# Performance work log

Measured on AMD Instinct MI355X. Metric: run time of the kernel, lower is better.

Reference implementation:

```python
import jax, jax.numpy as jnp
import numpy as np

DN = ('NCHW', 'OIHW', 'NCHW')

def _conv(x, w, b, pad):
    y = jax.lax.conv_general_dilated(x, w, (1, 1), pad, dimension_numbers=DN)
    return y + b[None, :, None, None]

def setup_inputs() -> dict:
    key = jax.random.key(0)
    ks = jax.random.split(key, 8)
    B, C, H, W = 8, 256, 64, 64
    C8 = C // 8
    return {
        'x': jax.random.normal(ks[0], (B, C, H, W), jnp.float32),
        'wq': jax.random.normal(ks[1], (C8, C, 1, 3), jnp.float32) * 0.02,
        'bq': jax.random.normal(ks[2], (C8,), jnp.float32) * 0.02,
        'wk': jax.random.normal(ks[3], (C8, C, 3, 1), jnp.float32) * 0.02,
        'bk': jax.random.normal(ks[4], (C8,), jnp.float32) * 0.02,
        'wv': jax.random.normal(ks[5], (C, C, 1, 1), jnp.float32) * 0.02,
        'bv': jax.random.normal(ks[6], (C,), jnp.float32) * 0.02,
        'gamma': jax.random.normal(ks[7], (1,), jnp.float32),
    }

def reference(x, wq, bq, wk, bk, wv, bv, gamma):
    B, C, H, W = x.shape
    N = H * W
    # q: (1,3) kernel, pad (0,1); k: (3,1) kernel, pad (1,0); v: 1x1
    q = _conv(x, wq, bq, [(0, 0), (1, 1)]).reshape(B, -1, N)  # B, C/8, N
    k = _conv(x, wk, bk, [(1, 1), (0, 0)]).reshape(B, -1, N)  # B, C/8, N
    v = _conv(x, wv, bv, [(0, 0), (0, 0)]).reshape(B, C, N)   # B, C, N
    affinity = jnp.einsum('bci,bcj->bij', q, k)               # B, N, N
    affinity = jax.nn.softmax(affinity, axis=-1)
    # weights = v @ affinity^T  ->  (B, C, N)
    weights = jnp.einsum('bcj,bij->bci', v, affinity).reshape(B, C, H, W)
    return gamma[0] * weights + x
```

## Files before the change

### kernel.cpp

```cpp
#include <hip/hip_runtime.h>
#include <math.h>

#define LOG2E 1.44269504f

typedef unsigned short us;
typedef __attribute__((ext_vector_type(8))) short bf16x8;
typedef __attribute__((ext_vector_type(4))) float f32x4;
typedef __attribute__((ext_vector_type(16))) float f32x16;

static __device__ __forceinline__ us f2bf(float f) {
  union { float f; unsigned u; } v; v.f = f;
  unsigned r = v.u + 0x7fffu + ((v.u >> 16) & 1u);
  return (us)(r >> 16);
}

__global__ __launch_bounds__(256) void prep_kernel(
    const float* __restrict__ x, const float* __restrict__ wq,
    const float* __restrict__ wk, const float* __restrict__ wv,
    us* __restrict__ xT, us* __restrict__ wqc, us* __restrict__ wkc,
    us* __restrict__ wvb) {
  __shared__ __align__(16) us lt[64 * 68];
  int bid = blockIdx.x;
  int tid = threadIdx.x;
  if (bid < 2048) {
    int b = bid >> 8, cb = (bid >> 6) & 3, nb = bid & 63;
    const float* xb = x + (((size_t)(b * 256 + cb * 64)) << 12);
    int nl = tid & 63, ch = tid >> 6;
#pragma unroll
    for (int p = 0; p < 16; p++) {
      int c = p * 4 + ch;
      lt[nl * 68 + c] = f2bf(xb[((size_t)c << 12) + (nb * 64 + nl)]);
    }
    __syncthreads();
    us* xTb = xT + (((size_t)b << 12) + nb * 64) * 256 + cb * 64;
    int cw = tid & 7, nr0 = tid >> 3;
#pragma unroll
    for (int p2 = 0; p2 < 2; p2++) {
      int nr = p2 * 32 + nr0;
      uint2 lo = *(const uint2*)&lt[nr * 68 + cw * 8];
      uint2 hi = *(const uint2*)&lt[nr * 68 + cw * 8 + 4];
      *(uint4*)&xTb[(size_t)nr * 256 + cw * 8] = make_uint4(lo.x, lo.y, hi.x, hi.y);
    }
  } else {
    int idx = (bid - 2048) * 256 + tid;
    if (idx < 24576) {
      int oc = idx / 768, r = idx % 768, t = r >> 8, ic = r & 255;
      wqc[idx] = f2bf(wq[(oc * 256 + ic) * 3 + t] * LOG2E);
    } else if (idx < 49152) {
      int j = idx - 24576;
      int oc = j / 768, r = j % 768, t = r >> 8, ic = r & 255;
      wkc[j] = f2bf(wk[(oc * 256 + ic) * 3 + t]);
    } else if (idx < 114688) {
      int j = idx - 49152;
      wvb[j] = f2bf(wv[j]);
    }
  }
}

__global__ __launch_bounds__(256) void conv_kernel(
    const us* __restrict__ xT, const us* __restrict__ wqc,
    const us* __restrict__ wkc, const float* __restrict__ bq,
    const float* __restrict__ bk, const us* __restrict__ wvb,
    const float* __restrict__ bv, us* __restrict__ qT, us* __restrict__ kT,
    us* __restrict__ vblk) {
  int tid = threadIdx.x, lane = tid & 63, w = tid >> 6;
  int l15 = lane & 15, quad = lane >> 4;
  if (blockIdx.x < 512) {
    int bid = blockIdx.x;
    int b = bid & 7, rt = bid >> 3;
    int n0 = rt * 64, y = rt;
    bool isq = (w < 2);
    int m0 = (w & 1) * 16;
    const us* wc = isq ? wqc : wkc;
    const us* xTb = xT + (((size_t)b << 12) * 256);
    f32x4 acc[4];
#pragma unroll
    for (int nt = 0; nt < 4; nt++) acc[nt] = (f32x4){0.f, 0.f, 0.f, 0.f};
#pragma unroll
    for (int t = 0; t < 3; t++) {
      bool killT = (!isq) && ((t == 0 && y == 0) || (t == 2 && y == 63));
      if (!killT) {
        int dn = isq ? (t - 1) : (t - 1) * 64;
#pragma unroll
        for (int k8 = 0; k8 < 8; k8++) {
          int kloc = t * 256 + k8 * 32 + quad * 8;
          bf16x8 af = *(const bf16x8*)(wc + (size_t)(m0 + l15) * 768 + kloc);
          int ic = k8 * 32 + quad * 8;
#pragma unroll
          for (int nt = 0; nt < 4; nt++) {
            int nl = nt * 16 + l15;
            int ns = n0 + nl + dn;
            ns = ns < 0 ? 0 : (ns > 4095 ? 4095 : ns);
            bf16x8 bf = *(const bf16x8*)(xTb + (size_t)ns * 256 + ic);
            if (isq && ((t == 0 && nl == 0) || (t == 2 && nl == 63)))
              bf = (bf16x8){0, 0, 0, 0, 0, 0, 0, 0};
            acc[nt] = __builtin_amdgcn_mfma_f32_16x16x32_bf16(af, bf, acc[nt], 0, 0, 0);
          }
        }
      }
    }
    const float* bias = isq ? bq : bk;
    float bsc = isq ? LOG2E : 1.0f;
    us* outp = (isq ? qT : kT) + (((size_t)b << 12) * 32);
    float b0 = bias[m0 + quad * 4 + 0] * bsc;
    float b1 = bias[m0 + quad * 4 + 1] * bsc;
    float b2 = bias[m0 + quad * 4 + 2] * bsc;
    float b3 = bias[m0 + quad * 4 + 3] * bsc;
#pragma unroll
    for (int nt = 0; nt < 4; nt++) {
      int n = n0 + nt * 16 + l15;
      unsigned lo = (unsigned)f2bf(acc[nt][0] + b0) | ((unsigned)f2bf(acc[nt][1] + b1) << 16);
      unsigned hi = (unsigned)f2bf(acc[nt][2] + b2) | ((unsigned)f2bf(acc[nt][3] + b3) << 16);
      *(uint2*)(outp + (size_t)n * 32 + m0 + quad * 4) = make_uint2(lo, hi);
    }
  } else {
    int bid = blockIdx.x - 512;
    int b = bid & 7, nt0 = bid >> 3;
    int n0 = nt0 * 64;
    const us* xTb = xT + (((size_t)b << 12) * 256);
    f32x4 acc[4][4];
#pragma unroll
    for (int ct = 0; ct < 4; ct++)
#pragma unroll
      for (int nt = 0; nt < 4; nt++) acc[ct][nt] = (f32x4){0.f, 0.f, 0.f, 0.f};
#pragma unroll
    for (int kk = 0; kk < 8; kk++) {
      bf16x8 bfr[4];
#pragma unroll
      for (int nt = 0; nt < 4; nt++)
        bfr[nt] = *(const bf16x8*)(xTb + (size_t)(n0 + nt * 16 + l15) * 256 + kk * 32 + quad * 8);
#pragma unroll
      for (int ct = 0; ct < 4; ct++) {
        bf16x8 af = *(const bf16x8*)(wvb + (size_t)(w * 64 + ct * 16 + l15) * 256 + kk * 32 + quad * 8);
#pragma unroll
        for (int nt = 0; nt < 4; nt++)
          acc[ct][nt] = __builtin_amdgcn_mfma_f32_16x16x32_bf16(af, bfr[nt], acc[ct][nt], 0, 0, 0);
      }
    }
    us* vb = vblk + ((size_t)b << 20);
#pragma unroll
    for (int ct = 0; ct < 4; ct++) {
#pragma unroll
      for (int r = 0; r < 4; r++) {
        int oc = w * 64 + ct * 16 + quad * 4 + r;
        float bvv = bv[oc];
#pragma unroll
        for (int nt = 0; nt < 4; nt++) {
          vb[((size_t)((n0 >> 4) + nt) * 256 + oc) * 16 + l15] = f2bf(acc[ct][nt][r] + bvv);
        }
      }
    }
  }
}

__global__ __launch_bounds__(512, 8) void attn_kernel(
    const float* __restrict__ x, const us* __restrict__ qT,
    const us* __restrict__ kT, const us* __restrict__ vblk,
    const float* __restrict__ gamma_p, float* __restrict__ out) {
  __shared__ __align__(16) us pb[2][32 * 72];
  __shared__ float lpart[4][32];

  int tid = threadIdx.x, lane = tid & 63, w = tid >> 6;
  int l15 = lane & 15, quad = lane >> 4;
  int l31 = lane & 31, h32 = lane >> 5;
  int iw = w & 1, jq = w >> 1;

  int bid = blockIdx.x;
  int b = bid & 7, i0 = (bid >> 3) * 32;

  const us* qTb = qT + (((size_t)b << 12) * 32);
  const us* kTb = kT + (((size_t)b << 12) * 32);
  const us* vbb = vblk + ((size_t)b << 20);

  bf16x8 qf = *(const bf16x8*)(qTb + (size_t)(i0 + iw * 16 + l15) * 32 + quad * 8);

  const us* kbase = kTb + (size_t)(jq * 16 + l15) * 32 + quad * 8;
  const us* vbase = vbb + (size_t)(w * 32 + l31) * 16 + h32 * 8;
  int pwi = (iw * 16 + l15) * 72 + jq * 16 + quad * 4;
  int pri = l31 * 72 + h32 * 8;

  float lr = 0.f;
  f32x4 s;
  f32x16 o;
#pragma unroll
  for (int rg = 0; rg < 16; rg++) o[rg] = 0.f;

  bf16x8 kX, kY;
  bf16x8 vf0, vf1, vf2, vf3;

#define PREK(N, KD)                                                            \
  do { KD = *(const bf16x8*)(kbase + (size_t)((N) & 63) * 2048); } while (0)

#define PREV(N)                                                                \
  do {                                                                         \
    const us* vp = vbase + (size_t)((N) & 63) * 16384;                         \
    vf0 = *(const bf16x8*)(vp);                                                \
    vf1 = *(const bf16x8*)(vp + 4096);                                         \
    vf2 = *(const bf16x8*)(vp + 8192);                                         \
    vf3 = *(const bf16x8*)(vp + 12288);                                        \
  } while (0)

#define STEP(N, KC, KN, BUF)                                                   \
  do {                                                                         \
    __builtin_amdgcn_s_setprio(1);                                             \
    s = __builtin_amdgcn_mfma_f32_16x16x32_bf16(KC, qf, (f32x4){0.f, 0.f, 0.f, 0.f}, 0, 0, 0); \
    __builtin_amdgcn_s_setprio(0);                                             \
    PREV(N);                                                                   \
    PREK((N) + 1, KN);                                                         \
    {                                                                          \
      float p0 = __builtin_amdgcn_exp2f(s[0]);                                 \
      float p1 = __builtin_amdgcn_exp2f(s[1]);                                 \
      float p2 = __builtin_amdgcn_exp2f(s[2]);                                 \
      float p3 = __builtin_amdgcn_exp2f(s[3]);                                 \
      lr += (p0 + p1) + (p2 + p3);                                             \
      unsigned e0, e1;                                                         \
      asm("v_cvt_pk_bf16_f32 %0, %1, %2" : "=v"(e0) : "v"(p0), "v"(p1));       \
      asm("v_cvt_pk_bf16_f32 %0, %1, %2" : "=v"(e1) : "v"(p2), "v"(p3));       \
      *(uint2*)((us*)pb + (BUF) * (32 * 72) + pwi) = make_uint2(e0, e1);       \
    }                                                                          \
    asm volatile("s_waitcnt lgkmcnt(0)" ::: "memory");                         \
    __builtin_amdgcn_s_barrier();                                              \
    __builtin_amdgcn_sched_barrier(0);                                         \
    {                                                                          \
      const us* pr = (const us*)pb + (BUF) * (32 * 72) + pri;                  \
      __builtin_amdgcn_s_setprio(1);                                           \
      bf16x8 pf;                                                               \
      pf = *(const bf16x8*)(pr + 0);                                           \
      o = __builtin_amdgcn_mfma_f32_32x32x16_bf16(vf0, pf, o, 0, 0, 0);        \
      pf = *(const bf16x8*)(pr + 16);                                          \
      o = __builtin_amdgcn_mfma_f32_32x32x16_bf16(vf1, pf, o, 0, 0, 0);        \
      pf = *(const bf16x8*)(pr + 32);                                          \
      o = __builtin_amdgcn_mfma_f32_32x32x16_bf16(vf2, pf, o, 0, 0, 0);        \
      pf = *(const bf16x8*)(pr + 48);                                          \
      o = __builtin_amdgcn_mfma_f32_32x32x16_bf16(vf3, pf, o, 0, 0, 0);        \
      __builtin_amdgcn_s_setprio(0);                                           \
    }                                                                          \
  } while (0)

  PREK(0, kX);
  for (int n2 = 0; n2 < 32; n2++) {
    STEP(2 * n2, kX, kY, 0);
    STEP(2 * n2 + 1, kY, kX, 1);
  }
#undef PREK
#undef PREV
#undef STEP

  float lt = lr;
  lt += __shfl_xor(lt, 16);
  lt += __shfl_xor(lt, 32);
  if (quad == 0) lpart[jq][iw * 16 + l15] = lt;
  __syncthreads();
  float g = gamma_p[0];
  const float* xb = x + ((size_t)b << 20);
  float* ob = out + ((size_t)b << 20);
  float gl = g / (lpart[0][l31] + lpart[1][l31] + lpart[2][l31] + lpart[3][l31]);
  int i = i0 + l31;
#pragma unroll
  for (int rg = 0; rg < 16; rg++) {
    int c = w * 32 + ((rg & 3) + 8 * (rg >> 2) + 4 * h32);
    size_t idx = ((size_t)c << 12) + i;
    ob[idx] = o[rg] * gl + xb[idx];
  }
}

extern "C" void kernel_launch(void* const* d_in, const int* in_sizes, int n_in,
                              void* d_out, int out_size, void* d_ws, size_t ws_size,
                              hipStream_t stream) {
  const float* x = (const float*)d_in[0];
  const float* wq = (const float*)d_in[1];
  const float* bq = (const float*)d_in[2];
  const float* wk = (const float*)d_in[3];
  const float* bk = (const float*)d_in[4];
  const float* wv = (const float*)d_in[5];
  const float* bv = (const float*)d_in[6];
  const float* gamma = (const float*)d_in[7];
  float* out = (float*)d_out;

  us* xT = (us*)d_ws;
  us* qT = xT + (size_t)8388608;
  us* kT = qT + (size_t)1048576;
  us* vblk = kT + (size_t)1048576;
  us* wqc = vblk + (size_t)8388608;
  us* wkc = wqc + (size_t)24576;
  us* wvb = wkc + (size_t)24576;

  prep_kernel<<<2496, 256, 0, stream>>>(x, wq, wk, wv, xT, wqc, wkc, wvb);
  conv_kernel<<<1024, 256, 0, stream>>>(xT, wqc, wkc, bq, bk, wvb, bv, qT, kT, vblk);
  attn_kernel<<<1024, 512, 0, stream>>>(x, qT, kT, vblk, gamma, out);
}
```

Baseline: 248.9 us.

## Double attention query tile per block and software-pipeline QK/PV across barriers

Each attention block now handles 64 query rows instead of 32. Each wave computes two QK tiles and two 32-channel output accumulators, so every V fragment and K fragment loaded from global memory is reused across twice as much work, and the grid is halved. The loop is restructured so the PV MFMAs for the previous tile overlap the QK and exp work of the current tile, with a single barrier per step. This raises register pressure, and the launch bound drops to 4 waves per SIMD, reducing occupancy.

New measurement: 242.1 us. 1.03x faster.

```diff
diff --git a/kernel.cpp b/kernel.cpp
--- a/kernel.cpp
+++ b/kernel.cpp
@@ -153,40 +153,42 @@
   }
 }
 
-__global__ __launch_bounds__(512, 8) void attn_kernel(
+__global__ __launch_bounds__(512, 4) void attn_kernel(
     const float* __restrict__ x, const us* __restrict__ qT,
     const us* __restrict__ kT, const us* __restrict__ vblk,
     const float* __restrict__ gamma_p, float* __restrict__ out) {
-  __shared__ __align__(16) us pb[2][32 * 72];
-  __shared__ float lpart[4][32];
+  __shared__ __align__(16) us pb[2][64 * 72];
+  __shared__ float lpart[4][64];
 
   int tid = threadIdx.x, lane = tid & 63, w = tid >> 6;
   int l15 = lane & 15, quad = lane >> 4;
   int l31 = lane & 31, h32 = lane >> 5;
-  int iw = w & 1, jq = w >> 1;
+  int jq = w & 3, ih = w >> 2;
+  int cq = w & 3, ihp = w >> 2;
 
   int bid = blockIdx.x;
-  int b = bid & 7, i0 = (bid >> 3) * 32;
+  int b = bid & 7, i0 = (bid >> 3) * 64;
 
   const us* qTb = qT + (((size_t)b << 12) * 32);
   const us* kTb = kT + (((size_t)b << 12) * 32);
   const us* vbb = vblk + ((size_t)b << 20);
 
-  bf16x8 qf = *(const bf16x8*)(qTb + (size_t)(i0 + iw * 16 + l15) * 32 + quad * 8);
+  bf16x8 qfa = *(const bf16x8*)(qTb + (size_t)(i0 + ih * 32 + l15) * 32 + quad * 8);
+  bf16x8 qfb = *(const bf16x8*)(qTb + (size_t)(i0 + ih * 32 + 16 + l15) * 32 + quad * 8);
 
   const us* kbase = kTb + (size_t)(jq * 16 + l15) * 32 + quad * 8;
-  const us* vbase = vbb + (size_t)(w * 32 + l31) * 16 + h32 * 8;
-  int pwi = (iw * 16 + l15) * 72 + jq * 16 + quad * 4;
-  int pri = l31 * 72 + h32 * 8;
-
-  float lr = 0.f;
-  f32x4 s;
-  f32x16 o;
-#pragma unroll
-  for (int rg = 0; rg < 16; rg++) o[rg] = 0.f;
+  const us* vbase = vbb + (size_t)(cq * 64 + l31) * 16 + h32 * 8;
+  int pwi = (ih * 32 + l15) * 72 + jq * 16 + quad * 4;
+  int pri = (ihp * 32 + l31) * 72 + h32 * 8;
+
+  float lr0 = 0.f, lr1 = 0.f;
+  f32x4 sa, sb;
+  f32x16 o0, o1;
+#pragma unroll
+  for (int rg = 0; rg < 16; rg++) { o0[rg] = 0.f; o1[rg] = 0.f; }
 
   bf16x8 kX, kY;
-  bf16x8 vf0, vf1, vf2, vf3;
+  bf16x8 va0, va1, va2, va3, vb0, vb1, vb2, vb3;
 
 #define PREK(N, KD)                                                            \
   do { KD = *(const bf16x8*)(kbase + (size_t)((N) & 63) * 2048); } while (0)
@@ -194,73 +196,138 @@
 #define PREV(N)                                                                \
   do {                                                                         \
     const us* vp = vbase + (size_t)((N) & 63) * 16384;                         \
-    vf0 = *(const bf16x8*)(vp);                                                \
-    vf1 = *(const bf16x8*)(vp + 4096);                                         \
-    vf2 = *(const bf16x8*)(vp + 8192);                                         \
-    vf3 = *(const bf16x8*)(vp + 12288);                                        \
-  } while (0)
-
-#define STEP(N, KC, KN, BUF)                                                   \
+    va0 = *(const bf16x8*)(vp);                                                \
+    vb0 = *(const bf16x8*)(vp + 512);                                          \
+    va1 = *(const bf16x8*)(vp + 4096);                                         \
+    vb1 = *(const bf16x8*)(vp + 4608);                                         \
+    va2 = *(const bf16x8*)(vp + 8192);                                         \
+    vb2 = *(const bf16x8*)(vp + 8704);                                         \
+    va3 = *(const bf16x8*)(vp + 12288);                                        \
+    vb3 = *(const bf16x8*)(vp + 12800);                                        \
+  } while (0)
+
+#define QKM(KC)                                                                \
   do {                                                                         \
     __builtin_amdgcn_s_setprio(1);                                             \
-    s = __builtin_amdgcn_mfma_f32_16x16x32_bf16(KC, qf, (f32x4){0.f, 0.f, 0.f, 0.f}, 0, 0, 0); \
+    sa = __builtin_amdgcn_mfma_f32_16x16x32_bf16(KC, qfa, (f32x4){0.f, 0.f, 0.f, 0.f}, 0, 0, 0); \
+    sb = __builtin_amdgcn_mfma_f32_16x16x32_bf16(KC, qfb, (f32x4){0.f, 0.f, 0.f, 0.f}, 0, 0, 0); \
     __builtin_amdgcn_s_setprio(0);                                             \
-    PREV(N);                                                                   \
-    PREK((N) + 1, KN);                                                         \
+  } while (0)
+
+#define PVM(BUF)                                                               \
+  do {                                                                         \
+    const us* pr = (const us*)pb + (BUF) * 4608 + pri;                         \
+    __builtin_amdgcn_s_setprio(1);                                             \
+    bf16x8 pf;                                                                 \
+    pf = *(const bf16x8*)(pr + 0);                                             \
+    o0 = __builtin_amdgcn_mfma_f32_32x32x16_bf16(va0, pf, o0, 0, 0, 0);        \
+    o1 = __builtin_amdgcn_mfma_f32_32x32x16_bf16(vb0, pf, o1, 0, 0, 0);        \
+    pf = *(const bf16x8*)(pr + 16);                                            \
+    o0 = __builtin_amdgcn_mfma_f32_32x32x16_bf16(va1, pf, o0, 0, 0, 0);        \
+    o1 = __builtin_amdgcn_mfma_f32_32x32x16_bf16(vb1, pf, o1, 0, 0, 0);        \
+    pf = *(const bf16x8*)(pr + 32);                                            \
+    o0 = __builtin_amdgcn_mfma_f32_32x32x16_bf16(va2, pf, o0, 0, 0, 0);        \
+    o1 = __builtin_amdgcn_mfma_f32_32x32x16_bf16(vb2, pf, o1, 0, 0, 0);        \
+    pf = *(const bf16x8*)(pr + 48);                                            \
+    o0 = __builtin_amdgcn_mfma_f32_32x32x16_bf16(va3, pf, o0, 0, 0, 0);        \
+    o1 = __builtin_amdgcn_mfma_f32_32x32x16_bf16(vb3, pf, o1, 0, 0, 0);        \
+    __builtin_amdgcn_s_setprio(0);                                             \
+  } while (0)
+
+#define SMW(BUF)                                                               \
+  do {                                                                         \
+    us* pw = (us*)pb + (BUF) * 4608 + pwi;                                     \
     {                                                                          \
-      float p0 = __builtin_amdgcn_exp2f(s[0]);                                 \
-      float p1 = __builtin_amdgcn_exp2f(s[1]);                                 \
-      float p2 = __builtin_amdgcn_exp2f(s[2]);                                 \
-      float p3 = __builtin_amdgcn_exp2f(s[3]);                                 \
-      lr += (p0 + p1) + (p2 + p3);                                             \
+      float p0 = __builtin_amdgcn_exp2f(sa[0]);                                \
+      float p1 = __builtin_amdgcn_exp2f(sa[1]);                                \
+      float p2 = __builtin_amdgcn_exp2f(sa[2]);                                \
+      float p3 = __builtin_amdgcn_exp2f(sa[3]);                                \
+      lr0 += (p0 + p1) + (p2 + p3);                                            \
       unsigned e0, e1;                                                         \
       asm("v_cvt_pk_bf16_f32 %0, %1, %2" : "=v"(e0) : "v"(p0), "v"(p1));       \
       asm("v_cvt_pk_bf16_f32 %0, %1, %2" : "=v"(e1) : "v"(p2), "v"(p3));       \
-      *(uint2*)((us*)pb + (BUF) * (32 * 72) + pwi) = make_uint2(e0, e1);       \
+      *(uint2*)pw = make_uint2(e0, e1);                                        \
     }                                                                          \
+    {                                                                          \
+      float p0 = __builtin_amdgcn_exp2f(sb[0]);                                \
+      float p1 = __builtin_amdgcn_exp2f(sb[1]);                                \
+      float p2 = __builtin_amdgcn_exp2f(sb[2]);                                \
+      float p3 = __builtin_amdgcn_exp2f(sb[3]);                                \
+      lr1 += (p0 + p1) + (p2 + p3);                                            \
+      unsigned e0, e1;                                                         \
+      asm("v_cvt_pk_bf16_f32 %0, %1, %2" : "=v"(e0) : "v"(p0), "v"(p1));       \
+      asm("v_cvt_pk_bf16_f32 %0, %1, %2" : "=v"(e1) : "v"(p2), "v"(p3));       \
+      *(uint2*)(pw + 1152) = make_uint2(e0, e1);                               \
+    }                                                                          \
+  } while (0)
+
+#define BAR                                                                    \
+  do {                                                                         \
     asm volatile("s_waitcnt lgkmcnt(0)" ::: "memory");                         \
     __builtin_amdgcn_s_barrier();                                              \
     __builtin_amdgcn_sched_barrier(0);                                         \
-    {                                                                          \
-      const us* pr = (const us*)pb + (BUF) * (32 * 72) + pri;                  \
-      __builtin_amdgcn_s_setprio(1);                                           \
-      bf16x8 pf;                                                               \
-      pf = *(const bf16x8*)(pr + 0);                                           \
-      o = __builtin_amdgcn_mfma_f32_32x32x16_bf16(vf0, pf, o, 0, 0, 0);        \
-      pf = *(const bf16x8*)(pr + 16);                                          \
-      o = __builtin_amdgcn_mfma_f32_32x32x16_bf16(vf1, pf, o, 0, 0, 0);        \
-      pf = *(const bf16x8*)(pr + 32);                                          \
-      o = __builtin_amdgcn_mfma_f32_32x32x16_bf16(vf2, pf, o, 0, 0, 0);        \
-      pf = *(const bf16x8*)(pr + 48);                                          \
-      o = __builtin_amdgcn_mfma_f32_32x32x16_bf16(vf3, pf, o, 0, 0, 0);        \
-      __builtin_amdgcn_s_setprio(0);                                           \
-    }                                                                          \
   } while (0)
 
   PREK(0, kX);
-  for (int n2 = 0; n2 < 32; n2++) {
-    STEP(2 * n2, kX, kY, 0);
-    STEP(2 * n2 + 1, kY, kX, 1);
-  }
+  PREK(1, kY);
+  QKM(kX);
+  PREV(0);
+  SMW(0);
+  BAR;
+  PREK(2, kX);
+  QKM(kY);
+  PVM(0);
+  PREV(1);
+  SMW(1);
+  BAR;
+  for (int jt2 = 1; jt2 < 32; jt2++) {
+    PREK(2 * jt2 + 1, kY);
+    QKM(kX);
+    PVM(1);
+    PREV(2 * jt2);
+    SMW(0);
+    BAR;
+    PREK(2 * jt2 + 2, kX);
+    QKM(kY);
+    PVM(0);
+    PREV(2 * jt2 + 1);
+    SMW(1);
+    BAR;
+  }
+  PVM(1);
+
 #undef PREK
 #undef PREV
-#undef STEP
-
-  float lt = lr;
-  lt += __shfl_xor(lt, 16);
-  lt += __shfl_xor(lt, 32);
-  if (quad == 0) lpart[jq][iw * 16 + l15] = lt;
+#undef QKM
+#undef PVM
+#undef SMW
+#undef BAR
+
+  float t0 = lr0, t1 = lr1;
+  t0 += __shfl_xor(t0, 16);
+  t0 += __shfl_xor(t0, 32);
+  t1 += __shfl_xor(t1, 16);
+  t1 += __shfl_xor(t1, 32);
+  if (quad == 0) {
+    lpart[jq][ih * 32 + l15] = t0;
+    lpart[jq][ih * 32 + 16 + l15] = t1;
+  }
   __syncthreads();
   float g = gamma_p[0];
   const float* xb = x + ((size_t)b << 20);
   float* ob = out + ((size_t)b << 20);
-  float gl = g / (lpart[0][l31] + lpart[1][l31] + lpart[2][l31] + lpart[3][l31]);
-  int i = i0 + l31;
-#pragma unroll
-  for (int rg = 0; rg < 16; rg++) {
-    int c = w * 32 + ((rg & 3) + 8 * (rg >> 2) + 4 * h32);
-    size_t idx = ((size_t)c << 12) + i;
-    ob[idx] = o[rg] * gl + xb[idx];
+  int il = ihp * 32 + l31;
+  float gl = g / (lpart[0][il] + lpart[1][il] + lpart[2][il] + lpart[3][il]);
+  int i = i0 + il;
+#pragma unroll
+  for (int ch = 0; ch < 2; ch++) {
+    const f32x16& o = (ch == 0) ? o0 : o1;
+#pragma unroll
+    for (int rg = 0; rg < 16; rg++) {
+      int c = cq * 64 + ch * 32 + ((rg & 3) + 8 * (rg >> 2) + 4 * h32);
+      size_t idx = ((size_t)c << 12) + i;
+      ob[idx] = o[rg] * gl + xb[idx];
+    }
   }
 }
 
@@ -287,5 +354,5 @@
 
   prep_kernel<<<2496, 256, 0, stream>>>(x, wq, wk, wv, xT, wqc, wkc, wvb);
   conv_kernel<<<1024, 256, 0, stream>>>(xT, wqc, wkc, bq, bk, wvb, bv, qT, kT, vblk);
-  attn_kernel<<<1024, 512, 0, stream>>>(x, qT, kT, vblk, gamma, out);
-}
+  attn_kernel<<<512, 512, 0, stream>>>(x, qT, kT, vblk, gamma, out);
+}
```
